# Optimization experiments

Hardware: AMD Instinct MI355X
Metric: run time of the kernel (lower is better)

Reference implementation:

```python
import jax, jax.numpy as jnp
import numpy as np

B, C, H, W = 32, 256, 32, 32   # batch, hidden_dim, latent grid
D, K = 256, 4096               # embedding_dim, num_embeddings
COMMITMENT_COST = 0.25


def setup_inputs() -> dict:
    key = jax.random.key(0)
    k1, k2, k3 = jax.random.split(key, 3)
    x = jax.random.normal(k1, (B, C, H, W), dtype=jnp.float32)
    conv_w = jax.random.normal(k2, (D, C), dtype=jnp.float32) * 0.02  # 1x1 conv kernel
    conv_b = jnp.zeros((D,), dtype=jnp.float32)
    # torch init: uniform_(-1/num_embeddings, 1/num_embeddings)
    emb = jax.random.uniform(k3, (K, D), dtype=jnp.float32,
                             minval=-1.0 / K, maxval=1.0 / K)
    return {"x": x, "conv_w": conv_w, "conv_b": conv_b, "emb": emb}


def reference(x, conv_w, conv_b, emb):
    # pre_vq_conv1: 1x1 conv == per-pixel matmul
    z = jnp.einsum('bchw,dc->bdhw', x, conv_w) + conv_b[None, :, None, None]
    inputs = jnp.transpose(z, (0, 2, 3, 1))            # [B,H,W,D]
    flat = inputs.reshape(-1, D)                       # [N,D]
    dist = (jnp.sum(flat * flat, axis=1, keepdims=True)
            + jnp.sum(emb * emb, axis=1)
            - 2.0 * flat @ emb.T)                      # [N,K]
    idx = jnp.argmin(dist, axis=1)                     # [N]
    # one-hot @ emb == direct gather
    quantized = emb[idx].reshape(inputs.shape)         # [B,H,W,D]
    sg = jax.lax.stop_gradient
    e_latent_loss = jnp.mean((sg(quantized) - inputs) ** 2)
    q_latent_loss = jnp.mean((quantized - sg(inputs)) ** 2)
    loss = q_latent_loss + COMMITMENT_COST * e_latent_loss
    # straight-through estimator
    quantized_st = inputs + sg(quantized - inputs)
    quantized_out = jnp.transpose(quantized_st, (0, 3, 1, 2))  # [B,D,H,W]
    # perplexity: mean one-hot == normalized code counts
    n = flat.shape[0]
    avg_probs = jnp.zeros((K,), dtype=jnp.float32).at[idx].add(1.0) / n
    perplexity = jnp.exp(-jnp.sum(avg_probs * jnp.log(avg_probs + 1e-10)))
    return quantized_out, loss, perplexity
```

## Files before the change

kernel.cpp:

```cpp
#include <hip/hip_runtime.h>
#include <math.h>

#define BB   32
#define CC   256
#define DD   256
#define KK   4096
#define HW   1024
#define NPIX 32768
#define NELE 8388608
#define EPS_REPAIR 1e-6f

typedef unsigned short ushort_t;
typedef __attribute__((ext_vector_type(8))) short short8;
typedef __attribute__((ext_vector_type(4))) float f32x4;

__device__ __forceinline__ unsigned short f2bf(float v) {
    union { float f; unsigned u; } c; c.f = v;
    unsigned r = c.u + 0x7FFFu + ((c.u >> 16) & 1u);
    return (unsigned short)(r >> 16);
}
__device__ __forceinline__ float bf2f(unsigned short b) {
    union { unsigned u; float f; } c; c.u = ((unsigned)b) << 16;
    return c.f;
}
__device__ __forceinline__ void gll16(const void* g, void* l) {
    __builtin_amdgcn_global_load_lds(
        (const __attribute__((address_space(1))) void*)g,
        (__attribute__((address_space(3))) void*)l, 16, 0, 0);
}

__global__ void k_packB(const float* __restrict__ emb, ushort_t* __restrict__ Bp,
                        float* __restrict__ e_norm, int* __restrict__ counts,
                        float* __restrict__ accum) {
    int k = blockIdx.x;
    int lane = threadIdx.x;
    if (lane == 0) counts[k] = 0;
    if (k == 0 && lane < 2) accum[lane] = 0.0f;
    float4 v = reinterpret_cast<const float4*>(emb + (size_t)k * DD)[lane];
    float s = v.x * v.x + v.y * v.y + v.z * v.z + v.w * v.w;
    float vv[4] = {v.x, v.y, v.z, v.w};
    ushort_t* row = Bp + (size_t)k * 768 + lane * 4;
    #pragma unroll
    for (int c = 0; c < 4; ++c) {
        unsigned short h = f2bf(vv[c]);
        unsigned short l = f2bf(vv[c] - bf2f(h));
        row[c] = h; row[256 + c] = h; row[512 + c] = l;
    }
    #pragma unroll
    for (int off = 32; off; off >>= 1) s += __shfl_down(s, off);
    if (lane == 0) e_norm[k] = s;
}

__global__ __launch_bounds__(256) void k_conv(const float* __restrict__ x,
                                              const float* __restrict__ w,
                                              const float* __restrict__ bias,
                                              ushort_t* __restrict__ A2) {
    __shared__ __align__(16) float xt[32][260];
    int t = threadIdx.x;
    int n0 = blockIdx.x * 32;
    int b = n0 >> 10, hw0 = n0 & 1023;
    const float* xb = x + (size_t)b * (CC * HW) + hw0;

    int p = t & 31, cg = t >> 5;
    #pragma unroll
    for (int it = 0; it < 32; ++it) {
        int c = it * 8 + cg;
        xt[p][c] = xb[c * HW + p];
    }
    __syncthreads();

    int d = t;
    float acc[32];
    float bv = bias[d];
    #pragma unroll
    for (int i = 0; i < 32; ++i) acc[i] = bv;

    const float4* wrow = reinterpret_cast<const float4*>(w + (size_t)d * CC);
    for (int c4 = 0; c4 < 64; ++c4) {
        float4 w4 = wrow[c4];
        #pragma unroll
        for (int pp = 0; pp < 32; ++pp) {
            float4 x4 = *reinterpret_cast<const float4*>(&xt[pp][c4 * 4]);
            acc[pp] = fmaf(w4.x, x4.x, acc[pp]);
            acc[pp] = fmaf(w4.y, x4.y, acc[pp]);
            acc[pp] = fmaf(w4.z, x4.z, acc[pp]);
            acc[pp] = fmaf(w4.w, x4.w, acc[pp]);
        }
    }
    #pragma unroll
    for (int pp = 0; pp < 32; ++pp) {
        float v = acc[pp];
        unsigned short h = f2bf(v);
        unsigned short l = f2bf(v - bf2f(h));
        ushort_t* arow = A2 + (size_t)(n0 + pp) * 512;
        arow[d] = h; arow[256 + d] = l;
    }
}

__global__ __launch_bounds__(256, 2) void k_mfma_top2(
    const ushort_t* __restrict__ A2,
    const ushort_t* __restrict__ Bp,
    const float* __restrict__ e_norm,
    float* __restrict__ tv1, int* __restrict__ ti1,
    float* __restrict__ tv2, int* __restrict__ ti2) {
    __shared__ __align__(16) short smem[2][2][128][64];

    const int t = threadIdx.x;
    const int xcd = blockIdx.x & 7, slot = blockIdx.x >> 3;
    const int ch = xcd >> 1;
    const int mb = ((xcd & 1) << 7) | slot;
    const int n0 = mb * 128, c0 = ch * 1024;
    const int w = t >> 6, lane = t & 63;
    const int wr = w >> 1, wc = w & 1;
    const int lr = lane & 15, lg = lane >> 4;

    const int srow = t >> 3;
    const int g    = t & 7;
    const int sg   = (g ^ (srow & 7)) * 8;

    const int rc0 = ((lg)     ^ (lr & 7)) * 8;
    const int rc1 = ((4 + lg) ^ (lr & 7)) * 8;

    float v1[4][4], v2r[4][4];
    int   i1[4][4], i2r[4][4];
    #pragma unroll
    for (int m = 0; m < 4; ++m)
        #pragma unroll
        for (int j = 0; j < 4; ++j) {
            v1[m][j] = 3.0e38f; v2r[m][j] = 3.0e38f;
            i1[m][j] = 0x7FFFFFFF; i2r[m][j] = 0x7FFFFFFF;
        }

    auto stage = [&](int buf, int sb, int kstep) {
        const int code0 = c0 + sb * 128;
        const int Acol = ((kstep < 8) ? kstep : kstep - 8) * 64;
        const int Bcol = kstep * 64;
        #pragma unroll
        for (int s = 0; s < 4; ++s) {
            const int r = srow + 32 * s;
            gll16(&A2[(size_t)(n0 + r) * 512 + Acol + sg], &smem[buf][0][r][g * 8]);
            gll16(&Bp[(size_t)(code0 + r) * 768 + Bcol + sg], &smem[buf][1][r][g * 8]);
        }
    };

    f32x4 acc[4][4];
    stage(0, 0, 0);
    __syncthreads();
    int cur = 0, sub = 0, ks = 0;
    while (true) {
        int nks = ks + 1, nsub = sub;
        if (nks == 12) { nks = 0; nsub = sub + 1; }
        if (nsub < 8) stage(cur ^ 1, nsub, nks);

        if (ks == 0) {
            const f32x4 vz = {0.f, 0.f, 0.f, 0.f};
            #pragma unroll
            for (int m = 0; m < 4; ++m)
                #pragma unroll
                for (int n = 0; n < 4; ++n) acc[m][n] = vz;
        }
        #pragma unroll
        for (int kk = 0; kk < 2; ++kk) {
            const int rc = kk ? rc1 : rc0;
            short8 a[4], b[4];
            #pragma unroll
            for (int m = 0; m < 4; ++m)
                a[m] = *reinterpret_cast<const short8*>(
                    &smem[cur][0][wr * 64 + m * 16 + lr][rc]);
            #pragma unroll
            for (int n = 0; n < 4; ++n)
                b[n] = *reinterpret_cast<const short8*>(
                    &smem[cur][1][wc * 64 + n * 16 + lr][rc]);
            #pragma unroll
            for (int m = 0; m < 4; ++m)
                #pragma unroll
                for (int n = 0; n < 4; ++n)
                    acc[m][n] = __builtin_amdgcn_mfma_f32_16x16x32_bf16(
                        a[m], b[n], acc[m][n], 0, 0, 0);
        }
        if (ks == 11) {
            const int code0 = c0 + sub * 128;
            #pragma unroll
            for (int n = 0; n < 4; ++n) {
                const int col = code0 + wc * 64 + n * 16 + lr;
                const float en = e_norm[col];
                #pragma unroll
                for (int m = 0; m < 4; ++m)
                    #pragma unroll
                    for (int j = 0; j < 4; ++j) {
                        const float s = fmaf(-2.0f, acc[m][n][j], en);
                        const bool b1 = s < v1[m][j];
                        const bool b2 = s < v2r[m][j];
                        v2r[m][j] = b1 ? v1[m][j] : (b2 ? s : v2r[m][j]);
                        i2r[m][j] = b1 ? i1[m][j] : (b2 ? col : i2r[m][j]);
                        v1[m][j]  = b1 ? s   : v1[m][j];
                        i1[m][j]  = b1 ? col : i1[m][j];
                    }
            }
        }
        __syncthreads();
        cur ^= 1; ks = nks; sub = nsub;
        if (sub == 8) break;
    }

    #pragma unroll
    for (int mask = 1; mask <= 8; mask <<= 1) {
        #pragma unroll
        for (int m = 0; m < 4; ++m)
            #pragma unroll
            for (int j = 0; j < 4; ++j) {
                const float ov1 = __shfl_xor(v1[m][j], mask);
                const int   oi1 = __shfl_xor(i1[m][j], mask);
                const float ov2 = __shfl_xor(v2r[m][j], mask);
                const int   oi2 = __shfl_xor(i2r[m][j], mask);
                const bool tb = (ov1 < v1[m][j]) || (ov1 == v1[m][j] && oi1 < i1[m][j]);
                const float w1 = tb ? ov1 : v1[m][j];  const int w1i = tb ? oi1 : i1[m][j];
                const float l1 = tb ? v1[m][j] : ov1;  const int l1i = tb ? i1[m][j] : oi1;
                const float c2 = tb ? ov2 : v2r[m][j]; const int c2i = tb ? oi2 : i2r[m][j];
                const bool t2b = (c2 < l1) || (c2 == l1 && c2i < l1i);
                v1[m][j] = w1; i1[m][j] = w1i;
                v2r[m][j] = t2b ? c2 : l1; i2r[m][j] = t2b ? c2i : l1i;
            }
    }
    float* mgv = (float*)&smem[0][0][0][0];
    int*   mgi = (int*)((char*)&smem[0][0][0][0] + 2048);
    if (lr == 0) {
        #pragma unroll
        for (int m = 0; m < 4; ++m)
            #pragma unroll
            for (int j = 0; j < 4; ++j) {
                const int r = wr * 64 + m * 16 + lg * 4 + j;
                mgv[(r * 2 + wc) * 2 + 0] = v1[m][j];  mgv[(r * 2 + wc) * 2 + 1] = v2r[m][j];
                mgi[(r * 2 + wc) * 2 + 0] = i1[m][j];  mgi[(r * 2 + wc) * 2 + 1] = i2r[m][j];
            }
    }
    __syncthreads();
    if (t < 128) {
        const float a1 = mgv[(t * 2 + 0) * 2 + 0], a2 = mgv[(t * 2 + 0) * 2 + 1];
        const int  ai1 = mgi[(t * 2 + 0) * 2 + 0], ai2 = mgi[(t * 2 + 0) * 2 + 1];
        const float b1 = mgv[(t * 2 + 1) * 2 + 0], b2 = mgv[(t * 2 + 1) * 2 + 1];
        const int  bi1 = mgi[(t * 2 + 1) * 2 + 0], bi2 = mgi[(t * 2 + 1) * 2 + 1];
        const bool tb = (b1 < a1) || (b1 == a1 && bi1 < ai1);
        const float w1 = tb ? b1 : a1;  const int w1i = tb ? bi1 : ai1;
        const float l1 = tb ? a1 : b1;  const int l1i = tb ? ai1 : bi1;
        const float c2 = tb ? b2 : a2;  const int c2i = tb ? bi2 : ai2;
        const bool t2b = (c2 < l1) || (c2 == l1 && c2i < l1i);
        const size_t o = (size_t)ch * NPIX + n0 + t;
        tv1[o] = w1; ti1[o] = w1i;
        tv2[o] = t2b ? c2 : l1; ti2[o] = t2b ? c2i : l1i;
    }
}

__global__ __launch_bounds__(256) void k_select(
    const float* __restrict__ tv1, const int* __restrict__ ti1,
    const float* __restrict__ tv2, const int* __restrict__ ti2,
    const ushort_t* __restrict__ A2, const float* __restrict__ emb,
    const float* __restrict__ e_norm, int* __restrict__ idx,
    int* __restrict__ counts) {
    const int n = blockIdx.x * 256 + threadIdx.x;
    float g1 = tv1[n], g2 = tv2[n];
    int  gi1 = ti1[n], gi2 = ti2[n];
    #pragma unroll
    for (int c = 1; c < 4; ++c) {
        const size_t o = (size_t)c * NPIX + n;
        const float b1 = tv1[o], b2 = tv2[o];
        const int  bi1 = ti1[o], bi2 = ti2[o];
        const bool tb = (b1 < g1) || (b1 == g1 && bi1 < gi1);
        const float w1 = tb ? b1 : g1;  const int w1i = tb ? bi1 : gi1;
        const float l1 = tb ? g1 : b1;  const int l1i = tb ? gi1 : bi1;
        const float c2 = tb ? b2 : g2;  const int c2i = tb ? bi2 : gi2;
        const bool t2b = (c2 < l1) || (c2 == l1 && c2i < l1i);
        g1 = w1; gi1 = w1i;
        g2 = t2b ? c2 : l1; gi2 = t2b ? c2i : l1i;
    }
    int best = gi1;
    if (g2 - g1 < EPS_REPAIR) {
        const ushort_t* za = A2 + (size_t)n * 512;
        const float4* e1 = reinterpret_cast<const float4*>(emb + (size_t)gi1 * DD);
        const float4* e2 = reinterpret_cast<const float4*>(emb + (size_t)gi2 * DD);
        float d1 = 0.f, d2 = 0.f;
        for (int q = 0; q < 64; ++q) {
            const float4 a1 = e1[q], a2 = e2[q];
            #pragma unroll
            for (int c = 0; c < 4; ++c) {
                const int d = q * 4 + c;
                const float z = bf2f(za[d]) + bf2f(za[256 + d]);
                const float ev1 = (&a1.x)[c], ev2 = (&a2.x)[c];
                d1 = fmaf(z, ev1, d1);
                d2 = fmaf(z, ev2, d2);
            }
        }
        const float s1 = e_norm[gi1] - 2.f * d1;
        const float s2 = e_norm[gi2] - 2.f * d2;
        best = (s2 < s1 || (s2 == s1 && gi2 < gi1)) ? gi2 : gi1;
    }
    idx[n] = best;
    atomicAdd(&counts[best], 1);
}

__global__ __launch_bounds__(256) void k_gather(const float* __restrict__ emb,
                                                const ushort_t* __restrict__ A2,
                                                const int* __restrict__ idx,
                                                float* __restrict__ out,
                                                float* __restrict__ accum) {
    __shared__ float qt[256][33];
    int t = threadIdx.x;
    int n0 = blockIdx.x * 32;
    int b = n0 >> 10, hw0 = n0 & 1023;

    float ss = 0.0f;
    for (int p = 0; p < 32; ++p) {
        int row = idx[n0 + p];
        float q = emb[(size_t)row * DD + t];
        const ushort_t* za = A2 + (size_t)(n0 + p) * 512;
        float z = bf2f(za[t]) + bf2f(za[256 + t]);
        float df = q - z;
        ss = fmaf(df, df, ss);
        qt[t][p] = q;
    }
    __syncthreads();

    int dg = t >> 5, p = t & 31;
    float* ob = out + (size_t)b * (DD * HW) + hw0;
    #pragma unroll
    for (int s = 0; s < 32; ++s) {
        int d = dg + 8 * s;
        ob[d * HW + p] = qt[d][p];
    }

    #pragma unroll
    for (int off = 32; off; off >>= 1) ss += __shfl_down(ss, off);
    __shared__ float wsum[4];
    if ((t & 63) == 0) wsum[t >> 6] = ss;
    __syncthreads();
    if (t == 0) atomicAdd(accum, wsum[0] + wsum[1] + wsum[2] + wsum[3]);
}

__global__ void k_final(const int* __restrict__ counts, const float* __restrict__ accum,
                        float* __restrict__ out_scalars) {
    int t = threadIdx.x;
    float s = 0.0f;
    #pragma unroll
    for (int q = 0; q < 16; ++q) {
        float p = (float)counts[t * 16 + q] * (1.0f / 32768.0f);
        s += p * logf(p + 1e-10f);
    }
    #pragma unroll
    for (int off = 32; off; off >>= 1) s += __shfl_down(s, off);
    __shared__ float wsum[4];
    if ((t & 63) == 0) wsum[t >> 6] = s;
    __syncthreads();
    if (t == 0) {
        float ent = wsum[0] + wsum[1] + wsum[2] + wsum[3];
        out_scalars[0] = accum[0] * (1.25f / (float)NELE);
        out_scalars[1] = expf(-ent);
    }
}

extern "C" void kernel_launch(void* const* d_in, const int* in_sizes, int n_in,
                              void* d_out, int out_size, void* d_ws, size_t ws_size,
                              hipStream_t stream) {
    const float* x    = (const float*)d_in[0];
    const float* w    = (const float*)d_in[1];
    const float* bias = (const float*)d_in[2];
    const float* emb  = (const float*)d_in[3];
    float* out = (float*)d_out;

    char* ws = (char*)d_ws;
    ushort_t* A2   = (ushort_t*)ws;
    ushort_t* Bp   = (ushort_t*)(ws + 33554432);
    float* e_norm  = (float*)(ws + 39845888);
    int*   idx     = (int*)  (ws + 39862272);
    int*   counts  = (int*)  (ws + 39993344);
    float* accum   = (float*)(ws + 40009728);
    float* tv1     = (float*)(ws + 40009984);
    int*   ti1     = (int*)  (ws + 40534272);
    float* tv2     = (float*)(ws + 41058560);
    int*   ti2     = (int*)  (ws + 41582848);

    k_packB    <<<KK,    64, 0, stream>>>(emb, Bp, e_norm, counts, accum);
    k_conv     <<<1024, 256, 0, stream>>>(x, w, bias, A2);
    k_mfma_top2<<<1024, 256, 0, stream>>>(A2, Bp, e_norm, tv1, ti1, tv2, ti2);
    k_select   <<<128,  256, 0, stream>>>(tv1, ti1, tv2, ti2, A2, emb, e_norm, idx, counts);
    k_gather   <<<1024, 256, 0, stream>>>(emb, A2, idx, out, accum);
    k_final    <<<1,    256, 0, stream>>>(counts, accum, out + NELE);
}
```

Measured before the change: 463.8 us.

## Triple-buffer MFMA distance GEMM with 512-thread tiles and algebraic loss

The distance GEMM kernel now uses 512-thread blocks over 256-row tiles, each loaded once per code chunk. It runs a three-stage LDS pipeline with explicit waitcnt and barrier control, and caches codebook norms in LDS. The loss is rebuilt algebraically as ||z||^2 (summed in the conv kernel) plus the best distance score (summed in the select kernel), so the gather kernel no longer rereads the activations. This trims memory traffic and sync stalls, but the algebraic loss may lose precision through cancellation.

```diff
diff --git a/kernel.cpp b/kernel.cpp
--- a/kernel.cpp
+++ b/kernel.cpp
@@ -54,7 +54,8 @@
 __global__ __launch_bounds__(256) void k_conv(const float* __restrict__ x,
                                               const float* __restrict__ w,
                                               const float* __restrict__ bias,
-                                              ushort_t* __restrict__ A2) {
+                                              ushort_t* __restrict__ A2,
+                                              float* __restrict__ accum) {
     __shared__ __align__(16) float xt[32][260];
     int t = threadIdx.x;
     int n0 = blockIdx.x * 32;
@@ -87,39 +88,61 @@
             acc[pp] = fmaf(w4.w, x4.w, acc[pp]);
         }
     }
+    float zs = 0.0f;
     #pragma unroll
     for (int pp = 0; pp < 32; ++pp) {
         float v = acc[pp];
+        zs = fmaf(v, v, zs);
         unsigned short h = f2bf(v);
         unsigned short l = f2bf(v - bf2f(h));
         ushort_t* arow = A2 + (size_t)(n0 + pp) * 512;
         arow[d] = h; arow[256 + d] = l;
     }
-}
-
-__global__ __launch_bounds__(256, 2) void k_mfma_top2(
+    #pragma unroll
+    for (int off = 32; off; off >>= 1) zs += __shfl_down(zs, off);
+    __shared__ float wsum[4];
+    if ((t & 63) == 0) wsum[t >> 6] = zs;
+    __syncthreads();
+    if (t == 0) atomicAdd(accum, wsum[0] + wsum[1] + wsum[2] + wsum[3]);
+}
+
+__global__ __launch_bounds__(512, 2) void k_mfma_top2(
     const ushort_t* __restrict__ A2,
     const ushort_t* __restrict__ Bp,
     const float* __restrict__ e_norm,
     float* __restrict__ tv1, int* __restrict__ ti1,
     float* __restrict__ tv2, int* __restrict__ ti2) {
-    __shared__ __align__(16) short smem[2][2][128][64];
+    __shared__ __align__(16) short As[3][256][64];
+    __shared__ __align__(16) short Bs[3][128][64];
+    __shared__ float en_lds[1024];
 
     const int t = threadIdx.x;
     const int xcd = blockIdx.x & 7, slot = blockIdx.x >> 3;
     const int ch = xcd >> 1;
-    const int mb = ((xcd & 1) << 7) | slot;
-    const int n0 = mb * 128, c0 = ch * 1024;
+    const int mb = ((xcd & 1) << 6) | slot;
+    const int n0 = mb * 256, c0 = ch * 1024;
     const int w = t >> 6, lane = t & 63;
     const int wr = w >> 1, wc = w & 1;
     const int lr = lane & 15, lg = lane >> 4;
 
+    const int sg   = t & 7;
     const int srow = t >> 3;
-    const int g    = t & 7;
-    const int sg   = (g ^ (srow & 7)) * 8;
-
-    const int rc0 = ((lg)     ^ (lr & 7)) * 8;
-    const int rc1 = ((4 + lg) ^ (lr & 7)) * 8;
+
+    auto stage = [&](int buf, int sub_, int ks_) {
+        const int Acol = ((ks_ < 8) ? ks_ : ks_ - 8) * 64;
+        const int Bcol = ks_ * 64;
+        const int q = (sg ^ (srow & 7)) << 3;
+        #pragma unroll
+        for (int s = 0; s < 4; ++s) {
+            const int r = srow + 64 * s;
+            gll16(&A2[(size_t)(n0 + r) * 512 + Acol + q], &As[buf][r][sg << 3]);
+        }
+        #pragma unroll
+        for (int s = 0; s < 2; ++s) {
+            const int r = srow + 64 * s;
+            gll16(&Bp[(size_t)(c0 + sub_ * 128 + r) * 768 + Bcol + q], &Bs[buf][r][sg << 3]);
+        }
+    };
 
     float v1[4][4], v2r[4][4];
     int   i1[4][4], i2r[4][4];
@@ -131,76 +154,76 @@
             i1[m][j] = 0x7FFFFFFF; i2r[m][j] = 0x7FFFFFFF;
         }
 
-    auto stage = [&](int buf, int sb, int kstep) {
-        const int code0 = c0 + sb * 128;
-        const int Acol = ((kstep < 8) ? kstep : kstep - 8) * 64;
-        const int Bcol = kstep * 64;
-        #pragma unroll
-        for (int s = 0; s < 4; ++s) {
-            const int r = srow + 32 * s;
-            gll16(&A2[(size_t)(n0 + r) * 512 + Acol + sg], &smem[buf][0][r][g * 8]);
-            gll16(&Bp[(size_t)(code0 + r) * 768 + Bcol + sg], &smem[buf][1][r][g * 8]);
-        }
-    };
+    if (t < 256) gll16(&e_norm[c0 + t * 4], &en_lds[t * 4]);
+    stage(0, 0, 0);
+    stage(1, 0, 1);
 
     f32x4 acc[4][4];
-    stage(0, 0, 0);
-    __syncthreads();
-    int cur = 0, sub = 0, ks = 0;
-    while (true) {
-        int nks = ks + 1, nsub = sub;
-        if (nks == 12) { nks = 0; nsub = sub + 1; }
-        if (nsub < 8) stage(cur ^ 1, nsub, nks);
-
-        if (ks == 0) {
-            const f32x4 vz = {0.f, 0.f, 0.f, 0.f};
-            #pragma unroll
-            for (int m = 0; m < 4; ++m)
-                #pragma unroll
-                for (int n = 0; n < 4; ++n) acc[m][n] = vz;
-        }
-        #pragma unroll
-        for (int kk = 0; kk < 2; ++kk) {
-            const int rc = kk ? rc1 : rc0;
-            short8 a[4], b[4];
-            #pragma unroll
-            for (int m = 0; m < 4; ++m)
-                a[m] = *reinterpret_cast<const short8*>(
-                    &smem[cur][0][wr * 64 + m * 16 + lr][rc]);
-            #pragma unroll
-            for (int n = 0; n < 4; ++n)
-                b[n] = *reinterpret_cast<const short8*>(
-                    &smem[cur][1][wc * 64 + n * 16 + lr][rc]);
-            #pragma unroll
-            for (int m = 0; m < 4; ++m)
-                #pragma unroll
-                for (int n = 0; n < 4; ++n)
-                    acc[m][n] = __builtin_amdgcn_mfma_f32_16x16x32_bf16(
-                        a[m], b[n], acc[m][n], 0, 0, 0);
-        }
-        if (ks == 11) {
-            const int code0 = c0 + sub * 128;
-            #pragma unroll
-            for (int n = 0; n < 4; ++n) {
-                const int col = code0 + wc * 64 + n * 16 + lr;
-                const float en = e_norm[col];
+    for (int sub = 0; sub < 8; ++sub) {
+        #pragma unroll
+        for (int ks = 0; ks < 12; ++ks) {
+            if (ks == 11 && sub == 7) { asm volatile("s_waitcnt vmcnt(0) lgkmcnt(0)" ::: "memory"); }
+            else                      { asm volatile("s_waitcnt vmcnt(6) lgkmcnt(0)" ::: "memory"); }
+            __builtin_amdgcn_s_barrier();
+            __builtin_amdgcn_sched_barrier(0);
+
+            if (ks + 2 < 12) {
+                stage((ks + 2) % 3, sub, ks + 2);
+            } else if (sub < 7) {
+                stage((ks + 2) % 3, sub + 1, ks + 2 - 12);
+            }
+
+            if (ks == 0) {
+                const f32x4 vz = {0.f, 0.f, 0.f, 0.f};
                 #pragma unroll
                 for (int m = 0; m < 4; ++m)
                     #pragma unroll
-                    for (int j = 0; j < 4; ++j) {
-                        const float s = fmaf(-2.0f, acc[m][n][j], en);
-                        const bool b1 = s < v1[m][j];
-                        const bool b2 = s < v2r[m][j];
-                        v2r[m][j] = b1 ? v1[m][j] : (b2 ? s : v2r[m][j]);
-                        i2r[m][j] = b1 ? i1[m][j] : (b2 ? col : i2r[m][j]);
-                        v1[m][j]  = b1 ? s   : v1[m][j];
-                        i1[m][j]  = b1 ? col : i1[m][j];
-                    }
-            }
-        }
-        __syncthreads();
-        cur ^= 1; ks = nks; sub = nsub;
-        if (sub == 8) break;
+                    for (int n = 0; n < 4; ++n) acc[m][n] = vz;
+            }
+            const int buf = ks % 3;
+            #pragma unroll
+            for (int kk = 0; kk < 2; ++kk) {
+                short8 a[4], b[4];
+                #pragma unroll
+                for (int m = 0; m < 4; ++m) {
+                    const int r = wr * 64 + m * 16 + lr;
+                    a[m] = *reinterpret_cast<const short8*>(
+                        &As[buf][r][((kk * 4 + lg) ^ (r & 7)) << 3]);
+                }
+                #pragma unroll
+                for (int n = 0; n < 4; ++n) {
+                    const int r = wc * 64 + n * 16 + lr;
+                    b[n] = *reinterpret_cast<const short8*>(
+                        &Bs[buf][r][((kk * 4 + lg) ^ (r & 7)) << 3]);
+                }
+                #pragma unroll
+                for (int m = 0; m < 4; ++m)
+                    #pragma unroll
+                    for (int n = 0; n < 4; ++n)
+                        acc[m][n] = __builtin_amdgcn_mfma_f32_16x16x32_bf16(
+                            a[m], b[n], acc[m][n], 0, 0, 0);
+            }
+            if (ks == 11) {
+                const int base = sub * 128 + wc * 64;
+                #pragma unroll
+                for (int n = 0; n < 4; ++n) {
+                    const float en = en_lds[base + n * 16 + lr];
+                    const int col = c0 + base + n * 16 + lr;
+                    #pragma unroll
+                    for (int m = 0; m < 4; ++m)
+                        #pragma unroll
+                        for (int j = 0; j < 4; ++j) {
+                            const float s = fmaf(-2.0f, acc[m][n][j], en);
+                            const bool b1 = s < v1[m][j];
+                            const bool b2 = s < v2r[m][j];
+                            v2r[m][j] = b1 ? v1[m][j] : (b2 ? s : v2r[m][j]);
+                            i2r[m][j] = b1 ? i1[m][j] : (b2 ? col : i2r[m][j]);
+                            v1[m][j]  = b1 ? s   : v1[m][j];
+                            i1[m][j]  = b1 ? col : i1[m][j];
+                        }
+                }
+            }
+        }
     }
 
     #pragma unroll
@@ -222,8 +245,9 @@
                 v2r[m][j] = t2b ? c2 : l1; i2r[m][j] = t2b ? c2i : l1i;
             }
     }
-    float* mgv = (float*)&smem[0][0][0][0];
-    int*   mgi = (int*)((char*)&smem[0][0][0][0] + 2048);
+    __syncthreads();
+    float* mgv = (float*)&As[0][0][0];
+    int*   mgi = (int*)((char*)&As[0][0][0] + 4096);
     if (lr == 0) {
         #pragma unroll
         for (int m = 0; m < 4; ++m)
@@ -235,7 +259,7 @@
             }
     }
     __syncthreads();
-    if (t < 128) {
+    if (t < 256) {
         const float a1 = mgv[(t * 2 + 0) * 2 + 0], a2 = mgv[(t * 2 + 0) * 2 + 1];
         const int  ai1 = mgi[(t * 2 + 0) * 2 + 0], ai2 = mgi[(t * 2 + 0) * 2 + 1];
         const float b1 = mgv[(t * 2 + 1) * 2 + 0], b2 = mgv[(t * 2 + 1) * 2 + 1];
@@ -256,8 +280,9 @@
     const float* __restrict__ tv2, const int* __restrict__ ti2,
     const ushort_t* __restrict__ A2, const float* __restrict__ emb,
     const float* __restrict__ e_norm, int* __restrict__ idx,
-    int* __restrict__ counts) {
-    const int n = blockIdx.x * 256 + threadIdx.x;
+    int* __restrict__ counts, float* __restrict__ accum) {
+    const int t = threadIdx.x;
+    const int n = blockIdx.x * 256 + t;
     float g1 = tv1[n], g2 = tv2[n];
     int  gi1 = ti1[n], gi2 = ti2[n];
     #pragma unroll
@@ -274,6 +299,7 @@
         g2 = t2b ? c2 : l1; gi2 = t2b ? c2i : l1i;
     }
     int best = gi1;
+    float sbest = g1;
     if (g2 - g1 < EPS_REPAIR) {
         const ushort_t* za = A2 + (size_t)n * 512;
         const float4* e1 = reinterpret_cast<const float4*>(emb + (size_t)gi1 * DD);
@@ -292,31 +318,31 @@
         }
         const float s1 = e_norm[gi1] - 2.f * d1;
         const float s2 = e_norm[gi2] - 2.f * d2;
-        best = (s2 < s1 || (s2 == s1 && gi2 < gi1)) ? gi2 : gi1;
+        const bool take2 = (s2 < s1 || (s2 == s1 && gi2 < gi1));
+        best  = take2 ? gi2 : gi1;
+        sbest = take2 ? s2 : s1;
     }
     idx[n] = best;
     atomicAdd(&counts[best], 1);
+    #pragma unroll
+    for (int off = 32; off; off >>= 1) sbest += __shfl_down(sbest, off);
+    __shared__ float wsum[4];
+    if ((t & 63) == 0) wsum[t >> 6] = sbest;
+    __syncthreads();
+    if (t == 0) atomicAdd(accum + 1, wsum[0] + wsum[1] + wsum[2] + wsum[3]);
 }
 
 __global__ __launch_bounds__(256) void k_gather(const float* __restrict__ emb,
-                                                const ushort_t* __restrict__ A2,
                                                 const int* __restrict__ idx,
-                                                float* __restrict__ out,
-                                                float* __restrict__ accum) {
+                                                float* __restrict__ out) {
     __shared__ float qt[256][33];
     int t = threadIdx.x;
     int n0 = blockIdx.x * 32;
     int b = n0 >> 10, hw0 = n0 & 1023;
 
-    float ss = 0.0f;
     for (int p = 0; p < 32; ++p) {
         int row = idx[n0 + p];
-        float q = emb[(size_t)row * DD + t];
-        const ushort_t* za = A2 + (size_t)(n0 + p) * 512;
-        float z = bf2f(za[t]) + bf2f(za[256 + t]);
-        float df = q - z;
-        ss = fmaf(df, df, ss);
-        qt[t][p] = q;
+        qt[t][p] = emb[(size_t)row * DD + t];
     }
     __syncthreads();
 
@@ -327,13 +353,6 @@
         int d = dg + 8 * s;
         ob[d * HW + p] = qt[d][p];
     }
-
-    #pragma unroll
-    for (int off = 32; off; off >>= 1) ss += __shfl_down(ss, off);
-    __shared__ float wsum[4];
-    if ((t & 63) == 0) wsum[t >> 6] = ss;
-    __syncthreads();
-    if (t == 0) atomicAdd(accum, wsum[0] + wsum[1] + wsum[2] + wsum[3]);
 }
 
 __global__ void k_final(const int* __restrict__ counts, const float* __restrict__ accum,
@@ -352,7 +371,7 @@
     __syncthreads();
     if (t == 0) {
         float ent = wsum[0] + wsum[1] + wsum[2] + wsum[3];
-        out_scalars[0] = accum[0] * (1.25f / (float)NELE);
+        out_scalars[0] = (accum[0] + accum[1]) * (1.25f / (float)NELE);
         out_scalars[1] = expf(-ent);
     }
 }
@@ -379,9 +398,9 @@
     int*   ti2     = (int*)  (ws + 41582848);
 
     k_packB    <<<KK,    64, 0, stream>>>(emb, Bp, e_norm, counts, accum);
-    k_conv     <<<1024, 256, 0, stream>>>(x, w, bias, A2);
-    k_mfma_top2<<<1024, 256, 0, stream>>>(A2, Bp, e_norm, tv1, ti1, tv2, ti2);
-    k_select   <<<128,  256, 0, stream>>>(tv1, ti1, tv2, ti2, A2, emb, e_norm, idx, counts);
-    k_gather   <<<1024, 256, 0, stream>>>(emb, A2, idx, out, accum);
+    k_conv     <<<1024, 256, 0, stream>>>(x, w, bias, A2, accum);
+    k_mfma_top2<<<512,  512, 0, stream>>>(A2, Bp, e_norm, tv1, ti1, tv2, ti2);
+    k_select   <<<128,  256, 0, stream>>>(tv1, ti1, tv2, ti2, A2, emb, e_norm, idx, counts, accum);
+    k_gather   <<<1024, 256, 0, stream>>>(emb, idx, out);
     k_final    <<<1,    256, 0, stream>>>(counts, accum, out + NELE);
 }
```

After: 509.1 us. +9.8%, slower.
